# Kernel optimization log

Hardware: AMD Instinct MI355X
Metric: run time of the kernel (lower is better)

Reference implementation:

```python
import jax, jax.numpy as jnp
import numpy as np

N = 100000      # nodes
E = 1600000     # edges
IN_DIM = 256
H = 128         # hidden_mlp == hidden_gnn
Z = 32          # latent_dim
HD = 128        # hidden_dec


def _lin(k, fan_in, fan_out):
    # torch nn.Linear default init: U(-1/sqrt(fan_in), 1/sqrt(fan_in))
    kw, kb = jax.random.split(k)
    lim = 1.0 / np.sqrt(fan_in)
    W = jax.random.uniform(kw, (fan_in, fan_out), jnp.float32, -lim, lim)
    b = jax.random.uniform(kb, (fan_out,), jnp.float32, -lim, lim)
    return W, b


def setup_inputs() -> dict:
    key = jax.random.key(0)
    ks = jax.random.split(key, 16)
    x = jax.random.normal(ks[0], (N, IN_DIM), jnp.float32)
    edge_index = jax.random.randint(ks[1], (2, E), 0, N, jnp.int64)
    edge_attr = jax.random.uniform(ks[2], (E,), jnp.float32)

    W1, b1 = _lin(ks[3], IN_DIM, H)       # encoder mlp layer 1
    W2, b2 = _lin(ks[4], H, H)            # encoder mlp layer 2
    Wrel1, brel1 = _lin(ks[5], H, H)      # gnn1 lin_rel
    Wroot1, _ = _lin(ks[6], H, H)         # gnn1 lin_root (no bias)
    Wrel2, brel2 = _lin(ks[7], H, H)      # gnn2 lin_rel
    Wroot2, _ = _lin(ks[8], H, H)         # gnn2 lin_root
    Wmu, bmu = _lin(ks[9], H, Z)
    Wlv, blv = _lin(ks[10], H, Z)
    Wd1, bd1 = _lin(ks[11], Z, HD)
    Wd2, bd2 = _lin(ks[12], HD, IN_DIM)
    eps = jax.random.normal(ks[13], (N, Z), jnp.float32)  # reparam noise (fixed)

    return dict(x=x, edge_index=edge_index, edge_attr=edge_attr,
                W1=W1, b1=b1, W2=W2, b2=b2,
                Wrel1=Wrel1, brel1=brel1, Wroot1=Wroot1,
                Wrel2=Wrel2, brel2=brel2, Wroot2=Wroot2,
                Wmu=Wmu, bmu=bmu, Wlv=Wlv, blv=blv,
                Wd1=Wd1, bd1=bd1, Wd2=Wd2, bd2=bd2, eps=eps)


def _graph_conv(h, src, dst, w, Wrel, brel, Wroot):
    # PyG GraphConv (aggr='add'): out_i = lin_rel(sum_{j->i} w_ji * h_j) + lin_root(h_i)
    msgs = h[src] * w[:, None]                       # [E, H] gather
    agg = jax.ops.segment_sum(msgs, dst, num_segments=N)  # [N, H] scatter-add
    return agg @ Wrel + brel + h @ Wroot


def reference(x, edge_index, edge_attr,
              W1, b1, W2, b2,
              Wrel1, brel1, Wroot1,
              Wrel2, brel2, Wroot2,
              Wmu, bmu, Wlv, blv,
              Wd1, bd1, Wd2, bd2, eps):
    src, dst = edge_index[0], edge_index[1]
    # encoder MLP
    h = jax.nn.relu(x @ W1 + b1)
    h = jax.nn.relu(h @ W2 + b2)
    # two GraphConv message-passing layers with ReLU
    h = jax.nn.relu(_graph_conv(h, src, dst, edge_attr, Wrel1, brel1, Wroot1))
    h = jax.nn.relu(_graph_conv(h, src, dst, edge_attr, Wrel2, brel2, Wroot2))
    # heads
    mu = h @ Wmu + bmu
    logvar = h @ Wlv + blv
    # reparameterize with fixed eps
    z = mu + eps * jnp.exp(0.5 * logvar)
    # decoder MLP
    x_recon = jax.nn.relu(z @ Wd1 + bd1) @ Wd2 + bd2
    return x_recon, mu, logvar, z
```

## Files before the change

kernel.cpp:

```cpp
#include <hip/hip_runtime.h>
#include <math.h>

#define NN 100000
#define EE 1600000
#define NB 1563

typedef _Float16 f16;
typedef __attribute__((ext_vector_type(2))) _Float16 f16x2;
typedef __attribute__((ext_vector_type(8))) _Float16 f16x8;
typedef __attribute__((ext_vector_type(4))) float f32x4;
typedef unsigned int u32;

__device__ __forceinline__ float frelu(float v){ return v > 0.f ? v : 0.f; }

__device__ __forceinline__ f32x4 mfma16(f16x8 a, f16x8 b, f32x4 c){
    return __builtin_amdgcn_mfma_f32_16x16x32_f16(a, b, c, 0, 0, 0);
}

__device__ __forceinline__ int2 nt_load_int2(const int2* p){
    long long v = __builtin_nontemporal_load((const long long*)p);
    int2 r; r.x = (int)(v & 0xFFFFFFFFll); r.y = (int)(v >> 32);
    return r;
}

__global__ __launch_bounds__(256) void hist_pack(const int* __restrict__ dst,
                                                 int* __restrict__ blockhist,
                                                 const float* __restrict__ W1,
                                                 const float* __restrict__ W2,
                                                 const float* __restrict__ Wrel1,
                                                 const float* __restrict__ Wroot1,
                                                 const float* __restrict__ Wrel2,
                                                 const float* __restrict__ Wroot2,
                                                 const float* __restrict__ Wd1,
                                                 const float* __restrict__ Wd2,
                                                 const float* __restrict__ Wmu,
                                                 const float* __restrict__ Wlv,
                                                 f16* __restrict__ pack)
{
    __shared__ int cntS[NB];
    const int t = threadIdx.x;
    if (blockIdx.x < 250) {
        const int blk = blockIdx.x;
        for (int i = t; i < NB; i += 256) cntS[i] = 0;
        __syncthreads();
        const int ebase = blk * 6400;
        #pragma unroll
        for (int i = 0; i < 25; i++) {
            int k = dst[ebase + i * 256 + t] >> 6;
            atomicAdd(&cntS[k], 1);
        }
        __syncthreads();
        for (int i = t; i < NB; i += 256)
            blockhist[blk * NB + i] = cntS[i];
        return;
    }
    int tt = (blockIdx.x - 250) * 256 + t;
    float v;
    if (tt < 32768) {
        int l = tt;
        int j = l & 7, lane = (l >> 3) & 63, ct = (l >> 9) & 7, kk = l >> 12;
        int k = kk * 32 + ((lane >> 4) << 3) + j, c = (ct << 4) + (lane & 15);
        v = W1[k * 128 + c];
    } else if (tt < 49152) {
        int l = tt - 32768;
        int j = l & 7, lane = (l >> 3) & 63, ct = (l >> 9) & 7, kk = l >> 12;
        int k = kk * 32 + ((lane >> 4) << 3) + j, c = (ct << 4) + (lane & 15);
        v = W2[k * 128 + c];
    } else if (tt < 81920) {
        int l = tt - 49152;
        int j = l & 7, lane = (l >> 3) & 63, ct = (l >> 9) & 7, kk = l >> 12;
        int k = kk * 32 + ((lane >> 4) << 3) + j, c = (ct << 4) + (lane & 15);
        v = (k < 128) ? Wrel1[k * 128 + c] : Wroot1[(k - 128) * 128 + c];
    } else if (tt < 114688) {
        int l = tt - 81920;
        int j = l & 7, lane = (l >> 3) & 63, ct = (l >> 9) & 7, kk = l >> 12;
        int k = kk * 32 + ((lane >> 4) << 3) + j, c = (ct << 4) + (lane & 15);
        v = (k < 128) ? Wrel2[k * 128 + c] : Wroot2[(k - 128) * 128 + c];
    } else if (tt < 118784) {
        int l = tt - 114688;
        int j = l & 7, lane = (l >> 3) & 63, ct = (l >> 9) & 7;
        int k = ((lane >> 4) << 3) + j, c = (ct << 4) + (lane & 15);
        v = Wd1[k * 128 + c];
    } else if (tt < 151552) {
        int l = tt - 118784;
        int j = l & 7, lane = (l >> 3) & 63, ct = (l >> 9) & 15, kk = l >> 13;
        int k = kk * 32 + ((lane >> 4) << 3) + j, c = (ct << 4) + (lane & 15);
        v = Wd2[k * 256 + c];
    } else {
        int l = tt - 151552;
        int j = l & 7, lane = (l >> 3) & 63, ct = (l >> 9) & 3, kk = l >> 11;
        int k = kk * 32 + ((lane >> 4) << 3) + j, c = (ct << 4) + (lane & 15);
        v = (c < 32) ? Wmu[k * 32 + c] : Wlv[k * 32 + (c - 32)];
    }
    pack[tt] = (f16)v;
}

__global__ __launch_bounds__(256) void colscan(int* __restrict__ blockhist,
                                               int* __restrict__ totals)
{
    __shared__ int lds[256];
    const int t = threadIdx.x, k = blockIdx.x;
    int v = (t < 250) ? blockhist[t * NB + k] : 0;
    lds[t] = v;
    __syncthreads();
    for (int off = 1; off < 256; off <<= 1) {
        int y = (t >= off) ? lds[t - off] : 0;
        __syncthreads();
        lds[t] += y;
        __syncthreads();
    }
    if (t < 250) blockhist[t * NB + k] = lds[t] - v;
    if (t == 255) totals[k] = lds[255];
}

__global__ __launch_bounds__(256) void scatter(const int* __restrict__ src,
                                               const int* __restrict__ dst,
                                               const float* __restrict__ ea,
                                               const int* __restrict__ totals,
                                               const int* __restrict__ blockhist,
                                               int* __restrict__ bs_g,
                                               int2* __restrict__ tmp)
{
    __shared__ int bsS[NB + 1];
    __shared__ int tmpS[256];
    __shared__ int carryS;
    __shared__ int prefS[NB];
    __shared__ int cntS[NB];
    const int t = threadIdx.x, blk = blockIdx.x;
    if (t == 0) carryS = 0;
    __syncthreads();
    for (int c = 0; c < 7; c++) {
        int idx = c * 256 + t;
        int val = (idx < NB) ? totals[idx] : 0;
        tmpS[t] = val;
        __syncthreads();
        for (int off = 1; off < 256; off <<= 1) {
            int y = (t >= off) ? tmpS[t - off] : 0;
            __syncthreads();
            tmpS[t] += y;
            __syncthreads();
        }
        if (idx < NB) bsS[idx] = carryS + tmpS[t] - val;
        __syncthreads();
        if (t == 255) carryS += tmpS[255];
        __syncthreads();
    }
    if (t == 0) bsS[NB] = carryS;
    for (int i = t; i < NB; i += 256) {
        prefS[i] = blockhist[blk * NB + i];
        cntS[i] = 0;
    }
    __syncthreads();
    if (blk == 0)
        for (int i = t; i < NB + 1; i += 256) bs_g[i] = bsS[i];
    const int ebase = blk * 6400;
    #pragma unroll
    for (int i = 0; i < 25; i++) {
        int e = ebase + i * 256 + t;
        int d = dst[e];
        int k = d >> 6;
        int rank = atomicAdd(&cntS[k], 1);
        int pos = bsS[k] + prefS[k] + rank;
        tmp[pos] = make_int2(src[e] | ((d & 63) << 17), __float_as_int(ea[e]));
    }
}

__global__ __launch_bounds__(256) void bucket_sort(const int2* __restrict__ tmp,
                                                   const int* __restrict__ bs_g,
                                                   int2* __restrict__ pairs,
                                                   int* __restrict__ offsets,
                                                   int* __restrict__ counts)
{
    __shared__ int hist[64], excl[64], cursor[64];
    const int t = threadIdx.x, k = blockIdx.x;
    const int start = bs_g[k], end = bs_g[k + 1];
    if (t < 64) hist[t] = 0;
    __syncthreads();
    for (int i = start + t; i < end; i += 256)
        atomicAdd(&hist[(tmp[i].x >> 17) & 63], 1);
    __syncthreads();
    if (t == 0) {
        int run = 0;
        #pragma unroll
        for (int j = 0; j < 64; j++) { excl[j] = run; cursor[j] = run; run += hist[j]; }
    }
    __syncthreads();
    for (int i = start + t; i < end; i += 256) {
        int2 e = tmp[i];
        int local = (e.x >> 17) & 63;
        int rank = atomicAdd(&cursor[local], 1);
        pairs[start + rank] = make_int2(e.x & 0x1FFFF, e.y);
    }
    if (t < 64) {
        int node = (k << 6) + t;
        if (node < NN) {
            counts[node]  = hist[t];
            offsets[node] = start + excl[t] + hist[t];
        }
    }
}

__global__ __launch_bounds__(256) void agg_q(const f16* __restrict__ h,
                                             const int2* __restrict__ pairs,
                                             const int* __restrict__ offsets,
                                             const int* __restrict__ counts,
                                             f16* __restrict__ out)
{
    const int gt   = blockIdx.x * 256 + threadIdx.x;
    const int node = gt >> 4;
    const int ch   = gt & 15;
    const int end  = offsets[node];
    int i = end - counts[node];
    float acc[8];
    #pragma unroll
    for (int j = 0; j < 8; j++) acc[j] = 0.f;
    const uint4* __restrict__ h16 = (const uint4*)h;
    for (; i + 2 <= end; i += 2) {
        int2 p0 = nt_load_int2(pairs + i);
        int2 p1 = nt_load_int2(pairs + i + 1);
        uint4 r0 = h16[(size_t)p0.x * 16 + ch];
        uint4 r1 = h16[(size_t)p1.x * 16 + ch];
        float w0 = __int_as_float(p0.y), w1 = __int_as_float(p1.y);
        const f16* e0 = (const f16*)&r0;
        const f16* e1 = (const f16*)&r1;
        #pragma unroll
        for (int j = 0; j < 8; j++) acc[j] = fmaf(w0, (float)e0[j], acc[j]);
        #pragma unroll
        for (int j = 0; j < 8; j++) acc[j] = fmaf(w1, (float)e1[j], acc[j]);
    }
    if (i < end) {
        int2 p0 = nt_load_int2(pairs + i);
        uint4 r0 = h16[(size_t)p0.x * 16 + ch];
        float w0 = __int_as_float(p0.y);
        const f16* e0 = (const f16*)&r0;
        #pragma unroll
        for (int j = 0; j < 8; j++) acc[j] = fmaf(w0, (float)e0[j], acc[j]);
    }
    union { f16 hh[8]; uint4 u; } cv;
    #pragma unroll
    for (int j = 0; j < 8; j++) cv.hh[j] = (f16)acc[j];
    ((uint4*)out)[(size_t)node * 16 + ch] = cv.u;
}

template<int C>
__device__ __forceinline__ void stage_tile(const float* __restrict__ src, int nbase,
                                           f16* lds, int ldr, int colofs)
{
    const int t = threadIdx.x;
    #pragma unroll
    for (int i = 0; i < (64 * C / 4) / 256; i++) {
        int elem = t + i * 256;
        int row = elem / (C / 4);
        int c4  = elem % (C / 4);
        int srow = nbase + row; if (srow >= NN) srow = NN - 1;
        float4 v = *(const float4*)(src + (size_t)srow * C + c4 * 4);
        union { f16 h[4]; uint2 u; } cv;
        cv.h[0] = (f16)v.x; cv.h[1] = (f16)v.y; cv.h[2] = (f16)v.z; cv.h[3] = (f16)v.w;
        *(uint2*)&lds[row * ldr + colofs + c4 * 4] = cv.u;
    }
}

template<int C>
__device__ __forceinline__ void stage_tile_f16(const f16* __restrict__ src, int nbase,
                                               f16* lds, int ldr, int colofs)
{
    const int t = threadIdx.x;
    #pragma unroll
    for (int i = 0; i < (64 * C / 4) / 256; i++) {
        int elem = t + i * 256;
        int row = elem / (C / 4);
        int c4  = elem % (C / 4);
        int srow = nbase + row; if (srow >= NN) srow = NN - 1;
        uint2 v = *(const uint2*)(src + (size_t)srow * C + c4 * 4);
        *(uint2*)&lds[row * ldr + colofs + c4 * 4] = v;
    }
}

template<int K, int CT>
__device__ __forceinline__ void wave_gemm(const f16* lds, int ldr,
                                          const f16x8* __restrict__ wp, f32x4 acc[CT])
{
    const int lane = threadIdx.x & 63;
    const int wrow = (threadIdx.x >> 6) * 16;
    const int arow = wrow + (lane & 15);
    const int kofs = (lane >> 4) << 3;
    #pragma unroll
    for (int kk = 0; kk < K / 32; kk++) {
        f16x8 a = *(const f16x8*)&lds[arow * ldr + kk * 32 + kofs];
        #pragma unroll
        for (int ct = 0; ct < CT; ct++) {
            f16x8 b = wp[(kk * CT + ct) * 64 + lane];
            acc[ct] = mfma16(a, b, acc[ct]);
        }
    }
}

template<int CT>
__device__ __forceinline__ void zacc(f32x4 acc[CT])
{
    #pragma unroll
    for (int ct = 0; ct < CT; ct++) acc[ct] = f32x4{0.f, 0.f, 0.f, 0.f};
}

template<int CT, bool RELU>
__device__ __forceinline__ void store_f32(float* __restrict__ dst, int OUTC, int nbase,
                                          const float* __restrict__ bias, f32x4 acc[CT])
{
    const int lane = threadIdx.x & 63;
    const int wrow = (threadIdx.x >> 6) * 16;
    #pragma unroll
    for (int ct = 0; ct < CT; ct++) {
        int c = ct * 16 + (lane & 15);
        float bv = bias[c];
        #pragma unroll
        for (int r = 0; r < 4; r++) {
            int node = nbase + wrow + ((lane >> 4) << 2) + r;
            if (node < NN) {
                float v = acc[ct][r] + bv;
                if (RELU) v = frelu(v);
                dst[(size_t)node * OUTC + c] = v;
            }
        }
    }
}

template<int CT, bool RELU>
__device__ __forceinline__ void store_f16g(f16* __restrict__ dst, int OUTC, int nbase,
                                           const float* __restrict__ bias, f32x4 acc[CT])
{
    const int lane = threadIdx.x & 63;
    const int wrow = (threadIdx.x >> 6) * 16;
    #pragma unroll
    for (int ct = 0; ct < CT; ct++) {
        int c = ct * 16 + (lane & 15);
        float bv = bias[c];
        #pragma unroll
        for (int r = 0; r < 4; r++) {
            int node = nbase + wrow + ((lane >> 4) << 2) + r;
            if (node < NN) {
                float v = acc[ct][r] + bv;
                if (RELU) v = frelu(v);
                dst[(size_t)node * OUTC + c] = (f16)v;
            }
        }
    }
}

template<int CT>
__device__ __forceinline__ void store_lds_f16(f16* lds, int ldr,
                                              const float* __restrict__ bias, f32x4 acc[CT])
{
    const int lane = threadIdx.x & 63;
    const int wrow = (threadIdx.x >> 6) * 16;
    #pragma unroll
    for (int ct = 0; ct < CT; ct++) {
        int c = ct * 16 + (lane & 15);
        float bv = bias[c];
        #pragma unroll
        for (int r = 0; r < 4; r++) {
            int row = wrow + ((lane >> 4) << 2) + r;
            lds[row * ldr + c] = (f16)frelu(acc[ct][r] + bv);
        }
    }
}

__global__ __launch_bounds__(256) void enc_mfma(const float* __restrict__ x,
                                                const f16x8* __restrict__ wp1,
                                                const f16x8* __restrict__ wp2,
                                                const float* __restrict__ b1,
                                                const float* __restrict__ b2,
                                                f16* __restrict__ out)
{
    __shared__ __align__(16) f16 xs[64 * 264];
    __shared__ __align__(16) f16 h1[64 * 136];
    const int nbase = blockIdx.x * 64;
    stage_tile<256>(x, nbase, xs, 264, 0);
    __syncthreads();
    f32x4 acc[8];
    zacc<8>(acc);
    wave_gemm<256, 8>(xs, 264, wp1, acc);
    store_lds_f16<8>(h1, 136, b1, acc);
    __syncthreads();
    zacc<8>(acc);
    wave_gemm<128, 8>(h1, 136, wp2, acc);
    store_f16g<8, true>(out, 128, nbase, b2, acc);
}

__global__ __launch_bounds__(256) void conv_mfma(const f16* __restrict__ agg,
                                                 const f16* __restrict__ h,
                                                 const f16x8* __restrict__ wp,
                                                 const float* __restrict__ brel,
                                                 f16* __restrict__ out)
{
    __shared__ __align__(16) f16 as_[64 * 264];
    const int nbase = blockIdx.x * 64;
    stage_tile_f16<128>(agg, nbase, as_, 264, 0);
    stage_tile_f16<128>(h,   nbase, as_, 264, 128);
    __syncthreads();
    f32x4 acc[8];
    zacc<8>(acc);
    wave_gemm<256, 8>(as_, 264, wp, acc);
    store_f16g<8, true>(out, 128, nbase, brel, acc);
}

__global__ __launch_bounds__(256) void tail_mfma(const f16* __restrict__ agg,
                                                 const f16* __restrict__ h,
                                                 const f16x8* __restrict__ wp_c2,
                                                 const float* __restrict__ brel2,
                                                 const f16x8* __restrict__ wp_hd,
                                                 const float* __restrict__ bmu,
                                                 const float* __restrict__ blv,
                                                 const f16x8* __restrict__ wp_d1,
                                                 const float* __restrict__ bd1,
                                                 const f16x8* __restrict__ wp_d2,
                                                 const float* __restrict__ bd2,
                                                 const float* __restrict__ eps,
                                                 float* __restrict__ out)
{
    __shared__ __align__(16) f16 as_[64 * 264];
    __shared__ __align__(16) f16 hd[64 * 136];
    __shared__ __align__(16) f16 zf[64 * 40];
    __shared__ __align__(16) float muS[64 * 32];
    __shared__ __align__(16) float lvS[64 * 32];
    const int nbase = blockIdx.x * 64;
    const int t = threadIdx.x;
    const int lane = t & 63;
    const int wrow = (t >> 6) * 16;

    stage_tile_f16<128>(agg, nbase, as_, 264, 0);
    stage_tile_f16<128>(h,   nbase, as_, 264, 128);
    __syncthreads();
    f32x4 acc8[8];
    zacc<8>(acc8);
    wave_gemm<256, 8>(as_, 264, wp_c2, acc8);
    __syncthreads();
    store_lds_f16<8>(as_, 136, brel2, acc8);
    __syncthreads();

    f32x4 acc4[4];
    zacc<4>(acc4);
    wave_gemm<128, 4>(as_, 136, wp_hd, acc4);
    #pragma unroll
    for (int ct = 0; ct < 4; ct++) {
        int c = ct * 16 + (lane & 15);
        bool ismu = (c < 32);
        int cc = c & 31;
        float bv = ismu ? bmu[cc] : blv[cc];
        float* gbase = out + (ismu ? (size_t)25600000 : (size_t)28800000);
        float* sb = ismu ? muS : lvS;
        #pragma unroll
        for (int r = 0; r < 4; r++) {
            int row = wrow + ((lane >> 4) << 2) + r;
            int node = nbase + row;
            float v = acc4[ct][r] + bv;
            sb[row * 32 + cc] = v;
            if (node < NN) gbase[(size_t)node * 32 + cc] = v;
        }
    }
    __syncthreads();

    {
        const int node = t >> 2;
        const int ch0  = (t & 3) * 8;
        const int gn = nbase + node;
        const float* mu = &muS[node * 32 + ch0];
        const float* lv = &lvS[node * 32 + ch0];
        float4 e0 = make_float4(0.f, 0.f, 0.f, 0.f), e1 = e0;
        if (gn < NN) {
            const size_t g = (size_t)gn * 32 + ch0;
            e0 = *(const float4*)(eps + g);
            e1 = *(const float4*)(eps + g + 4);
        }
        float zv[8];
        zv[0] = fmaf(e0.x, expf(0.5f * lv[0]), mu[0]);
        zv[1] = fmaf(e0.y, expf(0.5f * lv[1]), mu[1]);
        zv[2] = fmaf(e0.z, expf(0.5f * lv[2]), mu[2]);
        zv[3] = fmaf(e0.w, expf(0.5f * lv[3]), mu[3]);
        zv[4] = fmaf(e1.x, expf(0.5f * lv[4]), mu[4]);
        zv[5] = fmaf(e1.y, expf(0.5f * lv[5]), mu[5]);
        zv[6] = fmaf(e1.z, expf(0.5f * lv[6]), mu[6]);
        zv[7] = fmaf(e1.w, expf(0.5f * lv[7]), mu[7]);
        if (gn < NN) {
            const size_t g = (size_t)gn * 32 + ch0;
            *(float4*)(out + 32000000 + g)     = make_float4(zv[0], zv[1], zv[2], zv[3]);
            *(float4*)(out + 32000000 + g + 4) = make_float4(zv[4], zv[5], zv[6], zv[7]);
        }
        #pragma unroll
        for (int j = 0; j < 8; j++) zf[node * 40 + ch0 + j] = (f16)zv[j];
    }
    __syncthreads();

    f32x4 accd[8];
    zacc<8>(accd);
    wave_gemm<32, 8>(zf, 40, wp_d1, accd);
    store_lds_f16<8>(hd, 136, bd1, accd);
    __syncthreads();
    f32x4 acc16[16];
    zacc<16>(acc16);
    wave_gemm<128, 16>(hd, 136, wp_d2, acc16);
    store_f32<16, false>(out, 256, nbase, bd2, acc16);
}

extern "C" void kernel_launch(void* const* d_in, const int* in_sizes, int n_in,
                              void* d_out, int out_size, void* d_ws, size_t ws_size,
                              hipStream_t stream)
{
    const float* x     = (const float*)d_in[0];
    const int*   ei    = (const int*)d_in[1];
    const float* ea    = (const float*)d_in[2];
    const float* W1    = (const float*)d_in[3];
    const float* b1    = (const float*)d_in[4];
    const float* W2    = (const float*)d_in[5];
    const float* b2    = (const float*)d_in[6];
    const float* Wrel1 = (const float*)d_in[7];
    const float* brel1 = (const float*)d_in[8];
    const float* Wroot1= (const float*)d_in[9];
    const float* Wrel2 = (const float*)d_in[10];
    const float* brel2 = (const float*)d_in[11];
    const float* Wroot2= (const float*)d_in[12];
    const float* Wmu   = (const float*)d_in[13];
    const float* bmu   = (const float*)d_in[14];
    const float* Wlv   = (const float*)d_in[15];
    const float* blv   = (const float*)d_in[16];
    const float* Wd1   = (const float*)d_in[17];
    const float* bd1   = (const float*)d_in[18];
    const float* Wd2   = (const float*)d_in[19];
    const float* bd2   = (const float*)d_in[20];
    const float* eps   = (const float*)d_in[21];
    float* out = (float*)d_out;

    char* ws = (char*)d_ws;
    int*  totals    = (int*) (ws);
    int*  blockhist = (int*) (ws + 8192);
    int*  bs_g      = (int*) (ws + 1571200);
    int2* tmp       = (int2*)(ws + 1577472);
    int2* pairs     = (int2*)(ws + 14377472);
    int*  offsets   = (int*) (ws + 27177472);
    int*  counts    = (int*) (ws + 27577472);
    f16*  pack      = (f16*) (ws + 27977472);
    f16*  B0        = (f16*) (ws + 28300000);
    f16*  B1        = (f16*) (ws + 53900000);

    const f16x8* wp_enc1  = (const f16x8*)(pack);
    const f16x8* wp_enc2  = (const f16x8*)(pack + 32768);
    const f16x8* wp_conv1 = (const f16x8*)(pack + 49152);
    const f16x8* wp_conv2 = (const f16x8*)(pack + 81920);
    const f16x8* wp_dec1  = (const f16x8*)(pack + 114688);
    const f16x8* wp_dec2  = (const f16x8*)(pack + 118784);
    const f16x8* wp_heads = (const f16x8*)(pack + 151552);

    const int* src = ei;
    const int* dst = ei + EE;

    hist_pack<<<874, 256, 0, stream>>>(dst, blockhist, W1, W2, Wrel1, Wroot1,
                                       Wrel2, Wroot2, Wd1, Wd2, Wmu, Wlv, pack);
    colscan<<<NB, 256, 0, stream>>>(blockhist, totals);
    scatter<<<250, 256, 0, stream>>>(src, dst, ea, totals, blockhist, bs_g, tmp);
    bucket_sort<<<NB, 256, 0, stream>>>(tmp, bs_g, pairs, offsets, counts);

    enc_mfma<<<1563, 256, 0, stream>>>(x, wp_enc1, wp_enc2, b1, b2, B0);
    agg_q<<<6250, 256, 0, stream>>>(B0, pairs, offsets, counts, B1);
    conv_mfma<<<1563, 256, 0, stream>>>(B1, B0, wp_conv1, brel1, B1);
    agg_q<<<6250, 256, 0, stream>>>(B1, pairs, offsets, counts, B0);
    tail_mfma<<<1563, 256, 0, stream>>>(B0, B1, wp_conv2, brel2, wp_heads, bmu, blv,
                                        wp_dec1, bd1, wp_dec2, bd2, eps, out);
}
```

Before: 465.8 us.

## Merge column scan with encoder, split tail kernel, unroll aggregation by four

The colscan kernel and the encoder MLP are combined into one launch, with extra blocks running the encoder so it overlaps the scan and drops a kernel boundary. The second graph conv moves out of the fused tail into a separate conv_mfma launch, which shrinks tail LDS use and may raise occupancy, at the cost of one more global round trip for h. The aggregation loop now processes four edges per iteration to keep more gathers in flight. Workspace offsets for B0 and B1 shift slightly.

After: 397.2 us. 14.7% less time.

```diff
diff --git a/kernel.cpp b/kernel.cpp
--- a/kernel.cpp
+++ b/kernel.cpp
@@ -95,22 +95,168 @@
     pack[tt] = (f16)v;
 }
 
-__global__ __launch_bounds__(256) void colscan(int* __restrict__ blockhist,
-                                               int* __restrict__ totals)
-{
-    __shared__ int lds[256];
-    const int t = threadIdx.x, k = blockIdx.x;
-    int v = (t < 250) ? blockhist[t * NB + k] : 0;
-    lds[t] = v;
-    __syncthreads();
-    for (int off = 1; off < 256; off <<= 1) {
-        int y = (t >= off) ? lds[t - off] : 0;
+template<int C>
+__device__ __forceinline__ void stage_tile(const float* __restrict__ src, int nbase,
+                                           f16* lds, int ldr, int colofs)
+{
+    const int t = threadIdx.x;
+    #pragma unroll
+    for (int i = 0; i < (64 * C / 4) / 256; i++) {
+        int elem = t + i * 256;
+        int row = elem / (C / 4);
+        int c4  = elem % (C / 4);
+        int srow = nbase + row; if (srow >= NN) srow = NN - 1;
+        float4 v = *(const float4*)(src + (size_t)srow * C + c4 * 4);
+        union { f16 h[4]; uint2 u; } cv;
+        cv.h[0] = (f16)v.x; cv.h[1] = (f16)v.y; cv.h[2] = (f16)v.z; cv.h[3] = (f16)v.w;
+        *(uint2*)&lds[row * ldr + colofs + c4 * 4] = cv.u;
+    }
+}
+
+template<int C>
+__device__ __forceinline__ void stage_tile_f16(const f16* __restrict__ src, int nbase,
+                                               f16* lds, int ldr, int colofs)
+{
+    const int t = threadIdx.x;
+    #pragma unroll
+    for (int i = 0; i < (64 * C / 4) / 256; i++) {
+        int elem = t + i * 256;
+        int row = elem / (C / 4);
+        int c4  = elem % (C / 4);
+        int srow = nbase + row; if (srow >= NN) srow = NN - 1;
+        uint2 v = *(const uint2*)(src + (size_t)srow * C + c4 * 4);
+        *(uint2*)&lds[row * ldr + colofs + c4 * 4] = v;
+    }
+}
+
+template<int K, int CT>
+__device__ __forceinline__ void wave_gemm(const f16* lds, int ldr,
+                                          const f16x8* __restrict__ wp, f32x4 acc[CT])
+{
+    const int lane = threadIdx.x & 63;
+    const int wrow = (threadIdx.x >> 6) * 16;
+    const int arow = wrow + (lane & 15);
+    const int kofs = (lane >> 4) << 3;
+    #pragma unroll
+    for (int kk = 0; kk < K / 32; kk++) {
+        f16x8 a = *(const f16x8*)&lds[arow * ldr + kk * 32 + kofs];
+        #pragma unroll
+        for (int ct = 0; ct < CT; ct++) {
+            f16x8 b = wp[(kk * CT + ct) * 64 + lane];
+            acc[ct] = mfma16(a, b, acc[ct]);
+        }
+    }
+}
+
+template<int CT>
+__device__ __forceinline__ void zacc(f32x4 acc[CT])
+{
+    #pragma unroll
+    for (int ct = 0; ct < CT; ct++) acc[ct] = f32x4{0.f, 0.f, 0.f, 0.f};
+}
+
+template<int CT, bool RELU>
+__device__ __forceinline__ void store_f32(float* __restrict__ dst, int OUTC, int nbase,
+                                          const float* __restrict__ bias, f32x4 acc[CT])
+{
+    const int lane = threadIdx.x & 63;
+    const int wrow = (threadIdx.x >> 6) * 16;
+    #pragma unroll
+    for (int ct = 0; ct < CT; ct++) {
+        int c = ct * 16 + (lane & 15);
+        float bv = bias[c];
+        #pragma unroll
+        for (int r = 0; r < 4; r++) {
+            int node = nbase + wrow + ((lane >> 4) << 2) + r;
+            if (node < NN) {
+                float v = acc[ct][r] + bv;
+                if (RELU) v = frelu(v);
+                dst[(size_t)node * OUTC + c] = v;
+            }
+        }
+    }
+}
+
+template<int CT, bool RELU>
+__device__ __forceinline__ void store_f16g(f16* __restrict__ dst, int OUTC, int nbase,
+                                           const float* __restrict__ bias, f32x4 acc[CT])
+{
+    const int lane = threadIdx.x & 63;
+    const int wrow = (threadIdx.x >> 6) * 16;
+    #pragma unroll
+    for (int ct = 0; ct < CT; ct++) {
+        int c = ct * 16 + (lane & 15);
+        float bv = bias[c];
+        #pragma unroll
+        for (int r = 0; r < 4; r++) {
+            int node = nbase + wrow + ((lane >> 4) << 2) + r;
+            if (node < NN) {
+                float v = acc[ct][r] + bv;
+                if (RELU) v = frelu(v);
+                dst[(size_t)node * OUTC + c] = (f16)v;
+            }
+        }
+    }
+}
+
+template<int CT>
+__device__ __forceinline__ void store_lds_f16(f16* lds, int ldr,
+                                              const float* __restrict__ bias, f32x4 acc[CT])
+{
+    const int lane = threadIdx.x & 63;
+    const int wrow = (threadIdx.x >> 6) * 16;
+    #pragma unroll
+    for (int ct = 0; ct < CT; ct++) {
+        int c = ct * 16 + (lane & 15);
+        float bv = bias[c];
+        #pragma unroll
+        for (int r = 0; r < 4; r++) {
+            int row = wrow + ((lane >> 4) << 2) + r;
+            lds[row * ldr + c] = (f16)frelu(acc[ct][r] + bv);
+        }
+    }
+}
+
+__global__ __launch_bounds__(256) void colscan_enc(int* __restrict__ blockhist,
+                                                   int* __restrict__ totals,
+                                                   const float* __restrict__ x,
+                                                   const f16x8* __restrict__ wp1,
+                                                   const f16x8* __restrict__ wp2,
+                                                   const float* __restrict__ b1,
+                                                   const float* __restrict__ b2,
+                                                   f16* __restrict__ out)
+{
+    __shared__ __align__(16) f16 shbuf[64 * 264 + 64 * 136];
+    const int t = threadIdx.x;
+    if (blockIdx.x < NB) {
+        int* lds = (int*)shbuf;
+        const int k = blockIdx.x;
+        int v = (t < 250) ? blockhist[t * NB + k] : 0;
+        lds[t] = v;
         __syncthreads();
-        lds[t] += y;
-        __syncthreads();
-    }
-    if (t < 250) blockhist[t * NB + k] = lds[t] - v;
-    if (t == 255) totals[k] = lds[255];
+        for (int off = 1; off < 256; off <<= 1) {
+            int y = (t >= off) ? lds[t - off] : 0;
+            __syncthreads();
+            lds[t] += y;
+            __syncthreads();
+        }
+        if (t < 250) blockhist[t * NB + k] = lds[t] - v;
+        if (t == 255) totals[k] = lds[255];
+        return;
+    }
+    f16* xs = shbuf;
+    f16* h1 = shbuf + 64 * 264;
+    const int nbase = (blockIdx.x - NB) * 64;
+    stage_tile<256>(x, nbase, xs, 264, 0);
+    __syncthreads();
+    f32x4 acc[8];
+    zacc<8>(acc);
+    wave_gemm<256, 8>(xs, 264, wp1, acc);
+    store_lds_f16<8>(h1, 136, b1, acc);
+    __syncthreads();
+    zacc<8>(acc);
+    wave_gemm<128, 8>(h1, 136, wp2, acc);
+    store_f16g<8, true>(out, 128, nbase, b2, acc);
 }
 
 __global__ __launch_bounds__(256) void scatter(const int* __restrict__ src,
@@ -215,20 +361,31 @@
     #pragma unroll
     for (int j = 0; j < 8; j++) acc[j] = 0.f;
     const uint4* __restrict__ h16 = (const uint4*)h;
-    for (; i + 2 <= end; i += 2) {
+    for (; i + 4 <= end; i += 4) {
         int2 p0 = nt_load_int2(pairs + i);
         int2 p1 = nt_load_int2(pairs + i + 1);
+        int2 p2 = nt_load_int2(pairs + i + 2);
+        int2 p3 = nt_load_int2(pairs + i + 3);
         uint4 r0 = h16[(size_t)p0.x * 16 + ch];
         uint4 r1 = h16[(size_t)p1.x * 16 + ch];
+        uint4 r2 = h16[(size_t)p2.x * 16 + ch];
+        uint4 r3 = h16[(size_t)p3.x * 16 + ch];
         float w0 = __int_as_float(p0.y), w1 = __int_as_float(p1.y);
+        float w2 = __int_as_float(p2.y), w3 = __int_as_float(p3.y);
         const f16* e0 = (const f16*)&r0;
         const f16* e1 = (const f16*)&r1;
+        const f16* e2 = (const f16*)&r2;
+        const f16* e3 = (const f16*)&r3;
         #pragma unroll
         for (int j = 0; j < 8; j++) acc[j] = fmaf(w0, (float)e0[j], acc[j]);
         #pragma unroll
         for (int j = 0; j < 8; j++) acc[j] = fmaf(w1, (float)e1[j], acc[j]);
-    }
-    if (i < end) {
+        #pragma unroll
+        for (int j = 0; j < 8; j++) acc[j] = fmaf(w2, (float)e2[j], acc[j]);
+        #pragma unroll
+        for (int j = 0; j < 8; j++) acc[j] = fmaf(w3, (float)e3[j], acc[j]);
+    }
+    for (; i < end; ++i) {
         int2 p0 = nt_load_int2(pairs + i);
         uint4 r0 = h16[(size_t)p0.x * 16 + ch];
         float w0 = __int_as_float(p0.y);
@@ -240,150 +397,6 @@
     #pragma unroll
     for (int j = 0; j < 8; j++) cv.hh[j] = (f16)acc[j];
     ((uint4*)out)[(size_t)node * 16 + ch] = cv.u;
-}
-
-template<int C>
-__device__ __forceinline__ void stage_tile(const float* __restrict__ src, int nbase,
-                                           f16* lds, int ldr, int colofs)
-{
-    const int t = threadIdx.x;
-    #pragma unroll
-    for (int i = 0; i < (64 * C / 4) / 256; i++) {
-        int elem = t + i * 256;
-        int row = elem / (C / 4);
-        int c4  = elem % (C / 4);
-        int srow = nbase + row; if (srow >= NN) srow = NN - 1;
-        float4 v = *(const float4*)(src + (size_t)srow * C + c4 * 4);
-        union { f16 h[4]; uint2 u; } cv;
-        cv.h[0] = (f16)v.x; cv.h[1] = (f16)v.y; cv.h[2] = (f16)v.z; cv.h[3] = (f16)v.w;
-        *(uint2*)&lds[row * ldr + colofs + c4 * 4] = cv.u;
-    }
-}
-
-template<int C>
-__device__ __forceinline__ void stage_tile_f16(const f16* __restrict__ src, int nbase,
-                                               f16* lds, int ldr, int colofs)
-{
-    const int t = threadIdx.x;
-    #pragma unroll
-    for (int i = 0; i < (64 * C / 4) / 256; i++) {
-        int elem = t + i * 256;
-        int row = elem / (C / 4);
-        int c4  = elem % (C / 4);
-        int srow = nbase + row; if (srow >= NN) srow = NN - 1;
-        uint2 v = *(const uint2*)(src + (size_t)srow * C + c4 * 4);
-        *(uint2*)&lds[row * ldr + colofs + c4 * 4] = v;
-    }
-}
-
-template<int K, int CT>
-__device__ __forceinline__ void wave_gemm(const f16* lds, int ldr,
-                                          const f16x8* __restrict__ wp, f32x4 acc[CT])
-{
-    const int lane = threadIdx.x & 63;
-    const int wrow = (threadIdx.x >> 6) * 16;
-    const int arow = wrow + (lane & 15);
-    const int kofs = (lane >> 4) << 3;
-    #pragma unroll
-    for (int kk = 0; kk < K / 32; kk++) {
-        f16x8 a = *(const f16x8*)&lds[arow * ldr + kk * 32 + kofs];
-        #pragma unroll
-        for (int ct = 0; ct < CT; ct++) {
-            f16x8 b = wp[(kk * CT + ct) * 64 + lane];
-            acc[ct] = mfma16(a, b, acc[ct]);
-        }
-    }
-}
-
-template<int CT>
-__device__ __forceinline__ void zacc(f32x4 acc[CT])
-{
-    #pragma unroll
-    for (int ct = 0; ct < CT; ct++) acc[ct] = f32x4{0.f, 0.f, 0.f, 0.f};
-}
-
-template<int CT, bool RELU>
-__device__ __forceinline__ void store_f32(float* __restrict__ dst, int OUTC, int nbase,
-                                          const float* __restrict__ bias, f32x4 acc[CT])
-{
-    const int lane = threadIdx.x & 63;
-    const int wrow = (threadIdx.x >> 6) * 16;
-    #pragma unroll
-    for (int ct = 0; ct < CT; ct++) {
-        int c = ct * 16 + (lane & 15);
-        float bv = bias[c];
-        #pragma unroll
-        for (int r = 0; r < 4; r++) {
-            int node = nbase + wrow + ((lane >> 4) << 2) + r;
-            if (node < NN) {
-                float v = acc[ct][r] + bv;
-                if (RELU) v = frelu(v);
-                dst[(size_t)node * OUTC + c] = v;
-            }
-        }
-    }
-}
-
-template<int CT, bool RELU>
-__device__ __forceinline__ void store_f16g(f16* __restrict__ dst, int OUTC, int nbase,
-                                           const float* __restrict__ bias, f32x4 acc[CT])
-{
-    const int lane = threadIdx.x & 63;
-    const int wrow = (threadIdx.x >> 6) * 16;
-    #pragma unroll
-    for (int ct = 0; ct < CT; ct++) {
-        int c = ct * 16 + (lane & 15);
-        float bv = bias[c];
-        #pragma unroll
-        for (int r = 0; r < 4; r++) {
-            int node = nbase + wrow + ((lane >> 4) << 2) + r;
-            if (node < NN) {
-                float v = acc[ct][r] + bv;
-                if (RELU) v = frelu(v);
-                dst[(size_t)node * OUTC + c] = (f16)v;
-            }
-        }
-    }
-}
-
-template<int CT>
-__device__ __forceinline__ void store_lds_f16(f16* lds, int ldr,
-                                              const float* __restrict__ bias, f32x4 acc[CT])
-{
-    const int lane = threadIdx.x & 63;
-    const int wrow = (threadIdx.x >> 6) * 16;
-    #pragma unroll
-    for (int ct = 0; ct < CT; ct++) {
-        int c = ct * 16 + (lane & 15);
-        float bv = bias[c];
-        #pragma unroll
-        for (int r = 0; r < 4; r++) {
-            int row = wrow + ((lane >> 4) << 2) + r;
-            lds[row * ldr + c] = (f16)frelu(acc[ct][r] + bv);
-        }
-    }
-}
-
-__global__ __launch_bounds__(256) void enc_mfma(const float* __restrict__ x,
-                                                const f16x8* __restrict__ wp1,
-                                                const f16x8* __restrict__ wp2,
-                                                const float* __restrict__ b1,
-                                                const float* __restrict__ b2,
-                                                f16* __restrict__ out)
-{
-    __shared__ __align__(16) f16 xs[64 * 264];
-    __shared__ __align__(16) f16 h1[64 * 136];
-    const int nbase = blockIdx.x * 64;
-    stage_tile<256>(x, nbase, xs, 264, 0);
-    __syncthreads();
-    f32x4 acc[8];
-    zacc<8>(acc);
-    wave_gemm<256, 8>(xs, 264, wp1, acc);
-    store_lds_f16<8>(h1, 136, b1, acc);
-    __syncthreads();
-    zacc<8>(acc);
-    wave_gemm<128, 8>(h1, 136, wp2, acc);
-    store_f16g<8, true>(out, 128, nbase, b2, acc);
 }
 
 __global__ __launch_bounds__(256) void conv_mfma(const f16* __restrict__ agg,
@@ -403,43 +416,32 @@
     store_f16g<8, true>(out, 128, nbase, brel, acc);
 }
 
-__global__ __launch_bounds__(256) void tail_mfma(const f16* __restrict__ agg,
-                                                 const f16* __restrict__ h,
-                                                 const f16x8* __restrict__ wp_c2,
-                                                 const float* __restrict__ brel2,
-                                                 const f16x8* __restrict__ wp_hd,
-                                                 const float* __restrict__ bmu,
-                                                 const float* __restrict__ blv,
-                                                 const f16x8* __restrict__ wp_d1,
-                                                 const float* __restrict__ bd1,
-                                                 const f16x8* __restrict__ wp_d2,
-                                                 const float* __restrict__ bd2,
-                                                 const float* __restrict__ eps,
-                                                 float* __restrict__ out)
-{
-    __shared__ __align__(16) f16 as_[64 * 264];
-    __shared__ __align__(16) f16 hd[64 * 136];
-    __shared__ __align__(16) f16 zf[64 * 40];
+__global__ __launch_bounds__(256) void tail2_mfma(const f16* __restrict__ h,
+                                                  const f16x8* __restrict__ wp_hd,
+                                                  const float* __restrict__ bmu,
+                                                  const float* __restrict__ blv,
+                                                  const f16x8* __restrict__ wp_d1,
+                                                  const float* __restrict__ bd1,
+                                                  const f16x8* __restrict__ wp_d2,
+                                                  const float* __restrict__ bd2,
+                                                  const float* __restrict__ eps,
+                                                  float* __restrict__ out)
+{
+    __shared__ __align__(16) f16 hsA[64 * 136];
     __shared__ __align__(16) float muS[64 * 32];
     __shared__ __align__(16) float lvS[64 * 32];
+    __shared__ __align__(16) f16 zf[64 * 40];
     const int nbase = blockIdx.x * 64;
     const int t = threadIdx.x;
     const int lane = t & 63;
     const int wrow = (t >> 6) * 16;
 
-    stage_tile_f16<128>(agg, nbase, as_, 264, 0);
-    stage_tile_f16<128>(h,   nbase, as_, 264, 128);
-    __syncthreads();
-    f32x4 acc8[8];
-    zacc<8>(acc8);
-    wave_gemm<256, 8>(as_, 264, wp_c2, acc8);
-    __syncthreads();
-    store_lds_f16<8>(as_, 136, brel2, acc8);
+    stage_tile_f16<128>(h, nbase, hsA, 136, 0);
     __syncthreads();
 
     f32x4 acc4[4];
     zacc<4>(acc4);
-    wave_gemm<128, 4>(as_, 136, wp_hd, acc4);
+    wave_gemm<128, 4>(hsA, 136, wp_hd, acc4);
     #pragma unroll
     for (int ct = 0; ct < 4; ct++) {
         int c = ct * 16 + (lane & 15);
@@ -490,14 +492,15 @@
     }
     __syncthreads();
 
-    f32x4 accd[8];
-    zacc<8>(accd);
-    wave_gemm<32, 8>(zf, 40, wp_d1, accd);
-    store_lds_f16<8>(hd, 136, bd1, accd);
-    __syncthreads();
+    f32x4 acc8[8];
+    zacc<8>(acc8);
+    wave_gemm<32, 8>(zf, 40, wp_d1, acc8);
+    store_lds_f16<8>(hsA, 136, bd1, acc8);
+    __syncthreads();
+
     f32x4 acc16[16];
     zacc<16>(acc16);
-    wave_gemm<128, 16>(hd, 136, wp_d2, acc16);
+    wave_gemm<128, 16>(hsA, 136, wp_d2, acc16);
     store_f32<16, false>(out, 256, nbase, bd2, acc16);
 }
 
@@ -538,8 +541,8 @@
     int*  offsets   = (int*) (ws + 27177472);
     int*  counts    = (int*) (ws + 27577472);
     f16*  pack      = (f16*) (ws + 27977472);
-    f16*  B0        = (f16*) (ws + 28300000);
-    f16*  B1        = (f16*) (ws + 53900000);
+    f16*  B0        = (f16*) (ws + 28311552);
+    f16*  B1        = (f16*) (ws + 53911552);
 
     const f16x8* wp_enc1  = (const f16x8*)(pack);
     const f16x8* wp_enc2  = (const f16x8*)(pack + 32768);
@@ -554,14 +557,15 @@
 
     hist_pack<<<874, 256, 0, stream>>>(dst, blockhist, W1, W2, Wrel1, Wroot1,
                                        Wrel2, Wroot2, Wd1, Wd2, Wmu, Wlv, pack);
-    colscan<<<NB, 256, 0, stream>>>(blockhist, totals);
+    colscan_enc<<<NB + 1563, 256, 0, stream>>>(blockhist, totals, x,
+                                               wp_enc1, wp_enc2, b1, b2, B0);
     scatter<<<250, 256, 0, stream>>>(src, dst, ea, totals, blockhist, bs_g, tmp);
     bucket_sort<<<NB, 256, 0, stream>>>(tmp, bs_g, pairs, offsets, counts);
 
-    enc_mfma<<<1563, 256, 0, stream>>>(x, wp_enc1, wp_enc2, b1, b2, B0);
     agg_q<<<6250, 256, 0, stream>>>(B0, pairs, offsets, counts, B1);
     conv_mfma<<<1563, 256, 0, stream>>>(B1, B0, wp_conv1, brel1, B1);
     agg_q<<<6250, 256, 0, stream>>>(B1, pairs, offsets, counts, B0);
-    tail_mfma<<<1563, 256, 0, stream>>>(B0, B1, wp_conv2, brel2, wp_heads, bmu, blv,
-                                        wp_dec1, bd1, wp_dec2, bd2, eps, out);
-}
+    conv_mfma<<<1563, 256, 0, stream>>>(B0, B1, wp_conv2, brel2, B0);
+    tail2_mfma<<<1563, 256, 0, stream>>>(B0, wp_heads, bmu, blv,
+                                         wp_dec1, bd1, wp_dec2, bd2, eps, out);
+}
```
